# Kernel tuning notes

Measured on AMD Instinct MI355X. Metric: run time of the kernel, lower is better.

The kernel has to match this reference:

```python
import jax, jax.numpy as jnp
import numpy as np

D = 256
H = 8
HD = D // H
LN_EPS = 1e-5


def setup_inputs() -> dict:
    key = jax.random.key(0)
    ks = jax.random.split(key, 20)
    N = 768
    s = lambda *sh: 1.0 / np.sqrt(sh[-1])
    inp = {
        "features": jax.random.normal(ks[0], (N, D), jnp.float32),
        "boxes": jax.random.uniform(ks[1], (N, 4), jnp.float32),
        # MultiheadAttention params (torch layout: [out, in])
        "in_proj_w": jax.random.normal(ks[2], (3 * D, D), jnp.float32) * s(D),
        "in_proj_b": jnp.zeros((3 * D,), jnp.float32),
        "out_proj_w": jax.random.normal(ks[3], (D, D), jnp.float32) * s(D),
        "out_proj_b": jnp.zeros((D,), jnp.float32),
        # similarity_net params
        "w1": jax.random.normal(ks[4], (256, 3 * D + 3), jnp.float32) * s(3 * D + 3),
        "b1": jnp.zeros((256,), jnp.float32),
        "ln_g": jnp.ones((256,), jnp.float32),
        "ln_b": jnp.zeros((256,), jnp.float32),
        "w2": jax.random.normal(ks[5], (128, 256), jnp.float32) * s(256),
        "b2": jnp.zeros((128,), jnp.float32),
        "w3": jax.random.normal(ks[6], (64, 128), jnp.float32) * s(128),
        "b3": jnp.zeros((64,), jnp.float32),
        "w4": jax.random.normal(ks[7], (32, 64), jnp.float32) * s(64),
        "b4": jnp.zeros((32,), jnp.float32),
        "w5": jax.random.normal(ks[8], (1, 32), jnp.float32) * s(32),
        "b5": jnp.zeros((1,), jnp.float32),
    }
    return inp


def _mha(x, in_w, in_b, out_w, out_b):
    # x: [N, D]; torch nn.MultiheadAttention self-attention (eval mode)
    N = x.shape[0]
    qkv = x @ in_w.T + in_b                      # [N, 3D]
    q, k, v = jnp.split(qkv, 3, axis=-1)
    q = q.reshape(N, H, HD).transpose(1, 0, 2)   # [H, N, HD]
    k = k.reshape(N, H, HD).transpose(1, 0, 2)
    v = v.reshape(N, H, HD).transpose(1, 0, 2)
    scores = jnp.einsum("hnd,hmd->hnm", q, k) / np.sqrt(HD)
    attn = jax.nn.softmax(scores, axis=-1)
    o = jnp.einsum("hnm,hmd->hnd", attn, v)      # [H, N, HD]
    o = o.transpose(1, 0, 2).reshape(N, D)
    return o @ out_w.T + out_b


def reference(features, boxes, in_proj_w, in_proj_b, out_proj_w, out_proj_b,
              w1, b1, ln_g, ln_b, w2, b2, w3, b3, w4, b4, w5, b5):
    N = features.shape[0]
    att = _mha(features, in_proj_w, in_proj_b, out_proj_w, out_proj_b)  # [N, D]

    fi = jnp.broadcast_to(att[:, None, :], (N, N, D))
    fj = jnp.broadcast_to(att[None, :, :], (N, N, D))
    bi = boxes[:, None, :]
    bj = boxes[None, :, :]
    x_dist = jnp.abs(bi[:, :, 0] - bj[:, :, 0])
    y_diff = bi[:, :, 1] - bj[:, :, 1]
    spatial = jnp.stack([x_dist, jnp.abs(y_diff), y_diff], axis=-1)    # [N, N, 3]
    pairs = jnp.concatenate([fi, fj, fi * fj, spatial], axis=-1)       # [N, N, 3D+3]

    h = jax.nn.relu(pairs @ w1.T + b1)
    mu = jnp.mean(h, axis=-1, keepdims=True)
    var = jnp.var(h, axis=-1, keepdims=True)
    h = (h - mu) / jnp.sqrt(var + LN_EPS) * ln_g + ln_b
    h = jax.nn.relu(h @ w2.T + b2)
    h = jax.nn.relu(h @ w3.T + b3)
    h = jax.nn.relu(h @ w4.T + b4)
    logits = (h @ w5.T + b5)[..., 0]                                   # [N, N]

    eye = jnp.eye(N, dtype=logits.dtype)
    return logits * (1.0 - eye) - 1e9 * eye
```

## Files before the change

kernel.cpp:

```cpp
#include <hip/hip_runtime.h>


typedef __attribute__((ext_vector_type(8))) __bf16 bf16x8;
typedef __attribute__((ext_vector_type(4))) float f32x4;
typedef __attribute__((ext_vector_type(8))) int i32x8;

__device__ __forceinline__ float bf2f(unsigned short u) {
    return __uint_as_float(((unsigned int)u) << 16);
}
__device__ __forceinline__ unsigned short f2bf(float f) {
    union { __bf16 b; unsigned short u; } cv;
    cv.b = (__bf16)f;
    return cv.u;
}
__device__ __forceinline__ unsigned pk2(float lo, float hi) {
    return (unsigned)f2bf(lo) | ((unsigned)f2bf(hi) << 16);
}
__device__ __forceinline__ int pk4_fp8(float a, float b, float c, float d) {
    int w = __builtin_amdgcn_cvt_pk_fp8_f32(a, b, 0, false);
    w = __builtin_amdgcn_cvt_pk_fp8_f32(c, d, w, true);
    return w;
}
__device__ __forceinline__ unsigned char f2fp8(float v) {
    return (unsigned char)(__builtin_amdgcn_cvt_pk_fp8_f32(v, 0.f, 0, false) & 0xff);
}
__device__ __forceinline__ bf16x8 load8f_bf(const float* p) {
    float4 a = *reinterpret_cast<const float4*>(p);
    float4 b = *reinterpret_cast<const float4*>(p + 4);
    union { bf16x8 v; unsigned u[4]; } cv;
    cv.u[0] = pk2(a.x, a.y); cv.u[1] = pk2(a.z, a.w);
    cv.u[2] = pk2(b.x, b.y); cv.u[3] = pk2(b.z, b.w);
    return cv.v;
}
#define SC1 0x7F7F7F7F
#define MFMA_MX(a, b, c) __builtin_amdgcn_mfma_scale_f32_16x16x128_f8f6f4( \
        (a), (b), (c), 0, 0, 0, SC1, 0, SC1)

__global__ __launch_bounds__(256) void pack_all(
    const float* __restrict__ features, const float* __restrict__ in_proj_w,
    const float* __restrict__ in_proj_b, const float* __restrict__ out_proj_w,
    const float* __restrict__ w1, const float* __restrict__ w2,
    const float* __restrict__ w3, const float* __restrict__ w4,
    const float* __restrict__ b1, const float* __restrict__ ln_g,
    const float* __restrict__ ln_b, const float* __restrict__ b2,
    const float* __restrict__ out_proj_b,
    unsigned short* __restrict__ qkvb, unsigned short* __restrict__ Vt,
    unsigned short* __restrict__ WcatB,
    unsigned char* __restrict__ w1c_mx, unsigned char* __restrict__ w1t_f8,
    unsigned char* __restrict__ w2g_mx, unsigned char* __restrict__ w3_mx,
    unsigned char* __restrict__ w4_f8,
    float* __restrict__ bias768, float* __restrict__ c1, float* __restrict__ c2)
{
    const int blk = blockIdx.x;
    if (blk < 716) {
        int t = blk * 256 + threadIdx.x;
        if (t < 65536) {
            WcatB[t] = f2bf(out_proj_w[t]);
        } else if (t < 131072) {
            int u = t - 65536;
            int e = u & 31, lane = (u >> 5) & 63, f = u >> 11;
            int mt = f & 15, ks = f >> 4;
            int o = mt * 16 + (lane & 15);
            int k = ks * 128 + ((lane >> 4) & 3) * 32 + e;
            w1c_mx[u] = f2fp8(w1[o * 771 + 512 + k]);
        } else if (t < 139264) {
            int u = t - 131072;
            int e = u & 7, lane = (u >> 3) & 63, f = u >> 9;
            int o = f * 16 + (lane & 15);
            int k = ((lane >> 4) & 3) * 8 + e;
            float v = (k < 3) ? w1[o * 771 + 768 + k] : 0.f;
            w1t_f8[u] = f2fp8(v);
        } else if (t < 172032) {
            int u = t - 139264;
            int e = u & 31, lane = (u >> 5) & 63, f = u >> 11;
            int mt = f & 7, ks = f >> 3;
            int p = mt * 16 + (lane & 15);
            int k = ks * 128 + ((lane >> 4) & 3) * 32 + e;
            w2g_mx[u] = f2fp8(w2[p * 256 + k] * ln_g[k]);
        } else if (t < 180224) {
            int u = t - 172032;
            int e = u & 31, lane = (u >> 5) & 63, f = u >> 11;
            int o = f * 16 + (lane & 15);
            int k = ((lane >> 4) & 3) * 32 + e;
            w3_mx[u] = f2fp8(w3[o * 128 + k]);
        } else if (t < 182272) {
            int u = t - 180224;
            int e = u & 7, lane = (u >> 3) & 63, f = u >> 9;
            int l15 = lane & 15, quad = lane >> 4;
            int ct = f & 1, kc = f >> 1;
            int o = ct * 16 + l15, k = kc * 32 + quad * 8 + e;
            w4_f8[u] = f2fp8(w4[o * 64 + k]);
        } else if (t < 183040) {
            int n = t - 182272;
            if (n < 256) bias768[n] = out_proj_b[n];
            else {
                int m = n - 256;
                float s = 0.f;
                for (int d = 0; d < 256; d += 4) {
                    float4 ob = *reinterpret_cast<const float4*>(&out_proj_b[d]);
                    const float* wr = (m < 256) ? &w1[m * 771 + d]
                                                : &w1[(m - 256) * 771 + 256 + d];
                    float4 w = *reinterpret_cast<const float4*>(wr);
                    s += ob.x * w.x + ob.y * w.y + ob.z * w.z + ob.w * w.w;
                }
                bias768[n] = s + ((m < 256) ? b1[m] : 0.f);
            }
        } else if (t < 183168) {
            int p = t - 183040;
            float s2 = 0.f, s1 = 0.f;
            for (int k = 0; k < 256; k += 4) {
                float4 w = *reinterpret_cast<const float4*>(&w2[p * 256 + k]);
                float4 g = *reinterpret_cast<const float4*>(&ln_g[k]);
                float4 lb = *reinterpret_cast<const float4*>(&ln_b[k]);
                s2 += g.x * w.x + g.y * w.y + g.z * w.z + g.w * w.w;
                s1 += lb.x * w.x + lb.y * w.y + lb.z * w.z + lb.w * w.w;
            }
            c2[p] = s2;
            c1[p] = s1 + b2[p];
        }
    } else if (blk < 1228) {
        const int n = blk - 716, e = threadIdx.x;
        const float* wrow = (n < 256) ? &w1[n * 771] : &w1[(n - 256) * 771 + 256];
        float acc = 0.f;
        for (int d = 0; d < 256; d += 4) {
            float4 w = *reinterpret_cast<const float4*>(&wrow[d]);
            acc += w.x * out_proj_w[(d + 0) * 256 + e];
            acc += w.y * out_proj_w[(d + 1) * 256 + e];
            acc += w.z * out_proj_w[(d + 2) * 256 + e];
            acc += w.w * out_proj_w[(d + 3) * 256 + e];
        }
        WcatB[(256 + n) * 256 + e] = f2bf(acc);
    } else {
        const int q = blk - 1228;
        const int bm = q % 12, bn = q / 12;
        const int wv = threadIdx.x >> 6, lane = threadIdx.x & 63;
        const int l15 = lane & 15, quad = lane >> 4;
        const int row0 = bm * 64 + wv * 16;
        const int col0 = bn * 64;
        f32x4 acc[4] = {};
        for (int kc = 0; kc < 8; ++kc) {
            bf16x8 a = load8f_bf(&features[(row0 + l15) * 256 + kc * 32 + quad * 8]);
#pragma unroll
            for (int ct = 0; ct < 4; ++ct) {
                bf16x8 b = load8f_bf(&in_proj_w[(col0 + ct * 16 + l15) * 256 + kc * 32 + quad * 8]);
                acc[ct] = __builtin_amdgcn_mfma_f32_16x16x32_bf16(a, b, acc[ct], 0, 0, 0);
            }
        }
#pragma unroll
        for (int ct = 0; ct < 4; ++ct)
#pragma unroll
            for (int r = 0; r < 4; ++r) {
                int row = row0 + quad * 4 + r, col = col0 + ct * 16 + l15;
                float v = acc[ct][r] + in_proj_b[col];
                if (col < 512) qkvb[row * 768 + col] = f2bf(v);
                else           Vt[(col - 512) * 768 + row] = f2bf(v);
            }
    }
}

__global__ __launch_bounds__(256) void gemm_attab(
    const unsigned short* __restrict__ A, const unsigned short* __restrict__ W,
    const float* __restrict__ bias, float* __restrict__ att,
    float* __restrict__ AB)
{
    const int wv = threadIdx.x >> 6, lane = threadIdx.x & 63;
    const int l15 = lane & 15, quad = lane >> 4;
    const int row0 = blockIdx.x * 64 + wv * 16;
    const int col0 = blockIdx.y * 64;
    f32x4 acc[4] = {};
    for (int kc = 0; kc < 8; ++kc) {
        bf16x8 a = *reinterpret_cast<const bf16x8*>(&A[(row0 + l15) * 256 + kc * 32 + quad * 8]);
#pragma unroll
        for (int ct = 0; ct < 4; ++ct) {
            bf16x8 b = *reinterpret_cast<const bf16x8*>(&W[(col0 + ct * 16 + l15) * 256 + kc * 32 + quad * 8]);
            acc[ct] = __builtin_amdgcn_mfma_f32_16x16x32_bf16(a, b, acc[ct], 0, 0, 0);
        }
    }
#pragma unroll
    for (int ct = 0; ct < 4; ++ct)
#pragma unroll
        for (int r = 0; r < 4; ++r) {
            int row = row0 + quad * 4 + r, col = col0 + ct * 16 + l15;
            float v = acc[ct][r] + bias[col];
            if (col < 256) att[row * 256 + col] = v;
            else           AB[row * 512 + (col - 256)] = v;
        }
}

#define SP 776

__global__ __launch_bounds__(256) void attn_mfma(
    const unsigned short* __restrict__ qkvb, const unsigned short* __restrict__ Vt,
    unsigned short* __restrict__ Obf)
{
    __shared__ __align__(16) unsigned short smS[32 * SP];
    __shared__ float s_inv[32];
    const int h = blockIdx.x, q0 = blockIdx.y * 32, hb = h * 32;
    const int tid = threadIdx.x, wave = tid >> 6, lane = tid & 63;
    const int l15 = lane & 15, quad = lane >> 4;

    bf16x8 af[2];
#pragma unroll
    for (int mt = 0; mt < 2; ++mt)
        af[mt] = *reinterpret_cast<const bf16x8*>(&qkvb[(q0 + mt * 16 + l15) * 768 + hb + quad * 8]);
#pragma unroll
    for (int ct = 0; ct < 12; ++ct) {
        int n0 = wave * 192 + ct * 16;
        bf16x8 b = *reinterpret_cast<const bf16x8*>(&qkvb[(n0 + l15) * 768 + 256 + hb + quad * 8]);
#pragma unroll
        for (int mt = 0; mt < 2; ++mt) {
            f32x4 c = {};
            c = __builtin_amdgcn_mfma_f32_16x16x32_bf16(af[mt], b, c, 0, 0, 0);
#pragma unroll
            for (int r = 0; r < 4; ++r)
                smS[(mt * 16 + quad * 4 + r) * SP + n0 + l15] =
                    f2bf(c[r] * 0.17677669529663689f);
        }
    }
    __syncthreads();

    {
        const int row = tid >> 3, part = tid & 7;
        unsigned short* rp = &smS[row * SP + part * 96];
        float ls = 0.f;
#pragma unroll
        for (int c8 = 0; c8 < 12; ++c8) {
            uint4 v = *reinterpret_cast<const uint4*>(&rp[c8 * 8]);
            const unsigned short* pe = reinterpret_cast<const unsigned short*>(&v);
            unsigned short o8[8];
#pragma unroll
            for (int e = 0; e < 8; ++e) {
                float ev = __expf(bf2f(pe[e]));
                ls += ev;
                o8[e] = f2bf(ev);
            }
            *reinterpret_cast<uint4*>(&rp[c8 * 8]) = *reinterpret_cast<const uint4*>(o8);
        }
        ls += __shfl_xor(ls, 1, 64);
        ls += __shfl_xor(ls, 2, 64);
        ls += __shfl_xor(ls, 4, 64);
        if (part == 0) s_inv[row] = 1.0f / ls;
    }
    __syncthreads();

    const int row0 = (wave >> 1) * 16, cg = wave & 1;
    f32x4 accp = {};
    for (int kc = 0; kc < 24; ++kc) {
        bf16x8 a = *reinterpret_cast<const bf16x8*>(&smS[(row0 + l15) * SP + kc * 32 + quad * 8]);
        bf16x8 b = *reinterpret_cast<const bf16x8*>(&Vt[(hb + cg * 16 + l15) * 768 + kc * 32 + quad * 8]);
        accp = __builtin_amdgcn_mfma_f32_16x16x32_bf16(a, b, accp, 0, 0, 0);
    }
#pragma unroll
    for (int r = 0; r < 4; ++r) {
        int rloc = row0 + quad * 4 + r;
        Obf[(q0 + rloc) * 256 + hb + cg * 16 + l15] = f2bf(accp[r] * s_inv[rloc]);
    }
}

__global__ __launch_bounds__(512, 2) void pair_mlp(
    const float* __restrict__ att, const float* __restrict__ AB,
    const unsigned char* __restrict__ w1c_mx, const unsigned char* __restrict__ w1t_f8,
    const unsigned char* __restrict__ w2g_mx, const unsigned char* __restrict__ w3_mx,
    const unsigned char* __restrict__ w4_f8,
    const float* __restrict__ boxes,
    const float* __restrict__ c1, const float* __restrict__ c2,
    const float* __restrict__ b3, const float* __restrict__ b4,
    const float* __restrict__ w5, const float* __restrict__ b5,
    float* __restrict__ out)
{
    __shared__ __align__(16) unsigned char smH[64 * 384];
    __shared__ __align__(16) unsigned char smH1[64 * 256];
    __shared__ __align__(16) unsigned char smH2[64 * 192];
    __shared__ __align__(16) unsigned char smH3[64 * 72];
    __shared__ float s_psum[64][8], s_pssq[64][8];
    __shared__ float s_mu[64], s_rs[64];
    __shared__ float s_l5[64][2];

    const int i    = blockIdx.x;
    const int j0   = blockIdx.y * 64;
    const int tid  = threadIdx.x;
    const int wave = tid >> 6;
    const int lane = tid & 63;
    const int l15  = lane & 15;
    const int quad = lane >> 4;

    {
        const int g = tid & 63;
        const int ch = g >> 2;
        float4 fi4 = *reinterpret_cast<const float4*>(&att[i * 256 + g * 4]);
#pragma unroll 4
        for (int it = 0; it < 8; ++it) {
            int r = (tid >> 6) + it * 8;
            float4 aj = *reinterpret_cast<const float4*>(&att[(j0 + r) * 256 + g * 4]);
            int cs = ch ^ (r & 15);
            *reinterpret_cast<int*>(&smH[r * 384 + cs * 16 + (g & 3) * 4]) =
                pk4_fp8(aj.x * fi4.x, aj.y * fi4.y, aj.z * fi4.z, aj.w * fi4.w);
        }
    }
    if (tid < 64) {
        int j = j0 + tid;
        float xd = fabsf(boxes[i * 4 + 0] - boxes[j * 4 + 0]);
        float yd = boxes[i * 4 + 1] - boxes[j * 4 + 1];
        unsigned char* tb = &smH[tid * 384 + 256 + (tid & 3) * 24];
        *reinterpret_cast<int*>(tb)      = pk4_fp8(xd, fabsf(yd), yd, 0.f);
        *reinterpret_cast<int*>(tb + 4)  = 0;
        *reinterpret_cast<long long*>(tb + 8)  = 0;
        *reinterpret_cast<long long*>(tb + 16) = 0;
        *reinterpret_cast<long long*>(tb + 24) = 0;
    }
    __syncthreads();

    f32x4 acc1[2][4] = {};
#pragma unroll
    for (int ks = 0; ks < 2; ++ks) {
        i32x8 a0 = *reinterpret_cast<const i32x8*>(&w1c_mx[((ks * 16 + wave * 2 + 0) * 64 + lane) * 32]);
        i32x8 a1 = *reinterpret_cast<const i32x8*>(&w1c_mx[((ks * 16 + wave * 2 + 1) * 64 + lane) * 32]);
        const int cb = ks * 8 + quad * 2;
#pragma unroll
        for (int nt = 0; nt < 4; ++nt) {
            const unsigned char* rp = &smH[(nt * 16 + l15) * 384];
            union { i32x8 v; uint4 q[2]; } b;
            b.q[0] = *reinterpret_cast<const uint4*>(rp + ((cb    ) ^ l15) * 16);
            b.q[1] = *reinterpret_cast<const uint4*>(rp + ((cb + 1) ^ l15) * 16);
            acc1[0][nt] = MFMA_MX(a0, b.v, acc1[0][nt]);
            acc1[1][nt] = MFMA_MX(a1, b.v, acc1[1][nt]);
        }
    }
    {
        long long a0 = *reinterpret_cast<const long long*>(&w1t_f8[((wave * 2 + 0) * 64 + lane) * 8]);
        long long a1 = *reinterpret_cast<const long long*>(&w1t_f8[((wave * 2 + 1) * 64 + lane) * 8]);
#pragma unroll
        for (int nt = 0; nt < 4; ++nt) {
            long long b = *reinterpret_cast<const long long*>(
                &smH[(nt * 16 + l15) * 384 + 256 + (l15 & 3) * 24 + quad * 8]);
            acc1[0][nt] = __builtin_amdgcn_mfma_f32_16x16x32_fp8_fp8(a0, b, acc1[0][nt], 0, 0, 0);
            acc1[1][nt] = __builtin_amdgcn_mfma_f32_16x16x32_fp8_fp8(a1, b, acc1[1][nt], 0, 0, 0);
        }
    }

    const int o0 = wave * 32;
    float vsum[4] = {}, vssq[4] = {};
#pragma unroll
    for (int mt = 0; mt < 2; ++mt) {
        int o = o0 + mt * 16 + quad * 4;
        float4 Ai = *reinterpret_cast<const float4*>(&AB[i * 512 + o]);
        float AiA[4] = {Ai.x, Ai.y, Ai.z, Ai.w};
#pragma unroll
        for (int nt = 0; nt < 4; ++nt) {
            int j = nt * 16 + l15;
            float4 Bj = *reinterpret_cast<const float4*>(&AB[(j0 + j) * 512 + 256 + o]);
            float BjA[4] = {Bj.x, Bj.y, Bj.z, Bj.w};
#pragma unroll
            for (int r = 0; r < 4; ++r) {
                float v = fmaxf(acc1[mt][nt][r] + AiA[r] + BjA[r], 0.f);
                acc1[mt][nt][r] = v;
                vsum[nt] += v; vssq[nt] += v * v;
            }
        }
    }
#pragma unroll
    for (int nt = 0; nt < 4; ++nt) {
        vsum[nt] += __shfl_xor(vsum[nt], 16, 64);
        vsum[nt] += __shfl_xor(vsum[nt], 32, 64);
        vssq[nt] += __shfl_xor(vssq[nt], 16, 64);
        vssq[nt] += __shfl_xor(vssq[nt], 32, 64);
    }
    if (quad == 0)
#pragma unroll
        for (int nt = 0; nt < 4; ++nt) {
            s_psum[nt * 16 + l15][wave] = vsum[nt];
            s_pssq[nt * 16 + l15][wave] = vssq[nt];
        }
#pragma unroll
    for (int mt = 0; mt < 2; ++mt) {
        const int ch = wave * 2 + mt;
#pragma unroll
        for (int nt = 0; nt < 4; ++nt) {
            int j = nt * 16 + l15;
            *reinterpret_cast<int*>(&smH1[j * 256 + (ch ^ l15) * 16 + quad * 4]) =
                pk4_fp8(acc1[mt][nt][0], acc1[mt][nt][1], acc1[mt][nt][2], acc1[mt][nt][3]);
        }
    }
    __syncthreads();
    if (wave == 0) {
        int j = lane;
        float sm = 0.f, sq = 0.f;
#pragma unroll
        for (int w = 0; w < 8; ++w) { sm += s_psum[j][w]; sq += s_pssq[j][w]; }
        sm *= (1.0f / 256.0f); sq *= (1.0f / 256.0f);
        s_mu[j] = sm;
        s_rs[j] = rsqrtf(sq - sm * sm + 1e-5f);
    }

    f32x4 acc2[4] = {};
#pragma unroll
    for (int ks = 0; ks < 2; ++ks) {
        i32x8 a = *reinterpret_cast<const i32x8*>(&w2g_mx[((ks * 8 + wave) * 64 + lane) * 32]);
        const int cb = ks * 8 + quad * 2;
#pragma unroll
        for (int nt = 0; nt < 4; ++nt) {
            const unsigned char* rp = &smH1[(nt * 16 + l15) * 256];
            union { i32x8 v; uint4 q[2]; } b;
            b.q[0] = *reinterpret_cast<const uint4*>(rp + ((cb    ) ^ l15) * 16);
            b.q[1] = *reinterpret_cast<const uint4*>(rp + ((cb + 1) ^ l15) * 16);
            acc2[nt] = MFMA_MX(a, b.v, acc2[nt]);
        }
    }
    __syncthreads();
    {
        int p = wave * 16 + quad * 4;
        float4 C1 = *reinterpret_cast<const float4*>(&c1[p]);
        float4 C2 = *reinterpret_cast<const float4*>(&c2[p]);
        float C1A[4] = {C1.x, C1.y, C1.z, C1.w};
        float C2A[4] = {C2.x, C2.y, C2.z, C2.w};
#pragma unroll
        for (int nt = 0; nt < 4; ++nt) {
            int j = nt * 16 + l15;
            float mu = s_mu[j], rs = s_rs[j];
            float vv[4];
#pragma unroll
            for (int r = 0; r < 4; ++r)
                vv[r] = fmaxf(rs * (acc2[nt][r] - mu * C2A[r]) + C1A[r], 0.f);
            *reinterpret_cast<int*>(&smH2[j * 192 + (wave ^ (l15 & 7)) * 16 + quad * 4]) =
                pk4_fp8(vv[0], vv[1], vv[2], vv[3]);
        }
    }
    __syncthreads();

    const int qt  = wave >> 1;
    const int jh2 = wave & 1;
    f32x4 acc3[2] = {};
    {
        i32x8 a = *reinterpret_cast<const i32x8*>(&w3_mx[(qt * 64 + lane) * 32]);
        const int cb = quad * 2;
#pragma unroll
        for (int ntl = 0; ntl < 2; ++ntl) {
            int j = (jh2 * 2 + ntl) * 16 + l15;
            const unsigned char* rp = &smH2[j * 192];
            union { i32x8 v; uint4 q[2]; } b;
            b.q[0] = *reinterpret_cast<const uint4*>(rp + ((cb    ) ^ (l15 & 7)) * 16);
            b.q[1] = *reinterpret_cast<const uint4*>(rp + ((cb + 1) ^ (l15 & 7)) * 16);
            acc3[ntl] = MFMA_MX(a, b.v, acc3[ntl]);
        }
    }
    {
        int q = qt * 16 + quad * 4;
        float4 B3 = *reinterpret_cast<const float4*>(&b3[q]);
        float B3A[4] = {B3.x, B3.y, B3.z, B3.w};
#pragma unroll
        for (int ntl = 0; ntl < 2; ++ntl) {
            int j = (jh2 * 2 + ntl) * 16 + l15;
            float vv[4];
#pragma unroll
            for (int r = 0; r < 4; ++r)
                vv[r] = fmaxf(acc3[ntl][r] + B3A[r], 0.f);
            *reinterpret_cast<int*>(&smH3[j * 72 + q]) = pk4_fp8(vv[0], vv[1], vv[2], vv[3]);
        }
    }
    __syncthreads();

    const int mt4 = wave & 1;
    const int jq  = wave >> 1;
    f32x4 acc4 = {};
#pragma unroll
    for (int kc = 0; kc < 2; ++kc) {
        long long a = *reinterpret_cast<const long long*>(&w4_f8[((kc * 2 + mt4) * 64 + lane) * 8]);
        int j = jq * 16 + l15;
        long long b = *reinterpret_cast<const long long*>(&smH3[j * 72 + kc * 32 + quad * 8]);
        acc4 = __builtin_amdgcn_mfma_f32_16x16x32_fp8_fp8(a, b, acc4, 0, 0, 0);
    }
    {
        int o4 = mt4 * 16 + quad * 4;
        float4 B4 = *reinterpret_cast<const float4*>(&b4[o4]);
        float4 W5 = *reinterpret_cast<const float4*>(&w5[o4]);
        float B4A[4] = {B4.x, B4.y, B4.z, B4.w};
        float W5A[4] = {W5.x, W5.y, W5.z, W5.w};
        float part = 0.f;
#pragma unroll
        for (int r = 0; r < 4; ++r)
            part += fmaxf(acc4[r] + B4A[r], 0.f) * W5A[r];
        part += __shfl_xor(part, 16, 64);
        part += __shfl_xor(part, 32, 64);
        if (quad == 0)
            s_l5[jq * 16 + l15][mt4] = part;
    }
    __syncthreads();
    if (tid < 64) {
        int j = j0 + tid;
        float v = s_l5[tid][0] + s_l5[tid][1] + b5[0];
        out[i * 768 + j] = (j == i) ? -1.0e9f : v;
    }
}

extern "C" void kernel_launch(void* const* d_in, const int* in_sizes, int n_in,
                              void* d_out, int out_size, void* d_ws, size_t ws_size,
                              hipStream_t stream)
{
    const float* features   = (const float*)d_in[0];
    const float* boxes      = (const float*)d_in[1];
    const float* in_proj_w  = (const float*)d_in[2];
    const float* in_proj_b  = (const float*)d_in[3];
    const float* out_proj_w = (const float*)d_in[4];
    const float* out_proj_b = (const float*)d_in[5];
    const float* w1  = (const float*)d_in[6];
    const float* b1  = (const float*)d_in[7];
    const float* ln_g = (const float*)d_in[8];
    const float* ln_b = (const float*)d_in[9];
    const float* w2  = (const float*)d_in[10];
    const float* b2  = (const float*)d_in[11];
    const float* w3  = (const float*)d_in[12];
    const float* b3  = (const float*)d_in[13];
    const float* w4  = (const float*)d_in[14];
    const float* b4  = (const float*)d_in[15];
    const float* w5  = (const float*)d_in[16];
    const float* b5  = (const float*)d_in[17];
    float* out = (float*)d_out;

    char* p = (char*)d_ws;
    unsigned short* qkvb  = (unsigned short*)p; p += 768 * 768 * 2;
    unsigned short* Vt    = (unsigned short*)p; p += 256 * 768 * 2;
    unsigned short* Obf   = (unsigned short*)p; p += 768 * 256 * 2;
    unsigned short* WcatB = (unsigned short*)p; p += 196608 * 2;
    float* att = (float*)p; p += 768 * 256 * 4;
    float* AB  = (float*)p; p += 768 * 512 * 4;
    unsigned char* w1c_mx = (unsigned char*)p; p += 65536;
    unsigned char* w1t_f8 = (unsigned char*)p; p += 8192;
    unsigned char* w2g_mx = (unsigned char*)p; p += 32768;
    unsigned char* w3_mx  = (unsigned char*)p; p += 8192;
    unsigned char* w4_f8  = (unsigned char*)p; p += 2048;
    float* bias768 = (float*)p; p += 768 * 4;
    float* c1v     = (float*)p; p += 128 * 4;
    float* c2v     = (float*)p; p += 128 * 4;

    pack_all<<<dim3(1372), dim3(256), 0, stream>>>(features, in_proj_w,
        in_proj_b, out_proj_w, w1, w2, w3, w4, b1, ln_g, ln_b, b2, out_proj_b,
        qkvb, Vt, WcatB, w1c_mx, w1t_f8, w2g_mx, w3_mx, w4_f8,
        bias768, c1v, c2v);
    attn_mfma<<<dim3(8, 24), dim3(256), 0, stream>>>(qkvb, Vt, Obf);
    gemm_attab<<<dim3(12, 12), dim3(256), 0, stream>>>(Obf, WcatB, bias768,
        att, AB);
    pair_mlp<<<dim3(768, 12), dim3(512), 0, stream>>>(att, AB,
        w1c_mx, w1t_f8, w2g_mx, w3_mx, w4_f8, boxes, c1v, c2v,
        b3, b4, w5, b5, out);
}
```

Before: 283.1 us.

## Restructure pair MLP so each wave owns 32 pairs end-to-end without block syncs

The pair MLP kernel now runs 128-thread blocks in which each wave computes the full four-layer MLP for its own 32 j-columns. The layer-1 B operands are built directly in registers from global att instead of being staged in shared memory, and LayerNorm statistics are reduced inside the wave with shuffles. Only small per-wave shared buffers remain for the intermediate layers, which removes all __syncthreads and most LDS traffic. The cost is that every wave reloads the full weight matrices (more global/L2 traffic per pair), keeps larger accumulator arrays that raise register pressure, and issues redundant att loads per lane.

```diff
diff --git a/kernel.cpp b/kernel.cpp
--- a/kernel.cpp
+++ b/kernel.cpp
@@ -257,7 +257,7 @@
     }
 }
 
-__global__ __launch_bounds__(512, 2) void pair_mlp(
+__global__ __launch_bounds__(128, 3) void pair_mlp(
     const float* __restrict__ att, const float* __restrict__ AB,
     const unsigned char* __restrict__ w1c_mx, const unsigned char* __restrict__ w1t_f8,
     const unsigned char* __restrict__ w2g_mx, const unsigned char* __restrict__ w3_mx,
@@ -268,227 +268,215 @@
     const float* __restrict__ w5, const float* __restrict__ b5,
     float* __restrict__ out)
 {
-    __shared__ __align__(16) unsigned char smH[64 * 384];
-    __shared__ __align__(16) unsigned char smH1[64 * 256];
-    __shared__ __align__(16) unsigned char smH2[64 * 192];
-    __shared__ __align__(16) unsigned char smH3[64 * 72];
-    __shared__ float s_psum[64][8], s_pssq[64][8];
-    __shared__ float s_mu[64], s_rs[64];
-    __shared__ float s_l5[64][2];
-
-    const int i    = blockIdx.x;
-    const int j0   = blockIdx.y * 64;
-    const int tid  = threadIdx.x;
-    const int wave = tid >> 6;
-    const int lane = tid & 63;
-    const int l15  = lane & 15;
-    const int quad = lane >> 4;
-
+    __shared__ __align__(16) unsigned char smPool[2][8192];
+    const int tid = threadIdx.x, wave = tid >> 6, lane = tid & 63;
+    const int l15 = lane & 15, quad = lane >> 4;
+    const int i = blockIdx.x;
+    const int j0w = blockIdx.y * 64 + wave * 32;
+
+    unsigned char* const h1 = smPool[wave];
+    unsigned char* const h2 = smPool[wave];
+    unsigned char* const h3 = smPool[wave] + 4096;
+
+    i32x8 bf[2][2];
+    long long tf[2];
+#pragma unroll
+    for (int ks = 0; ks < 2; ++ks) {
+        const int bk = ks * 128 + quad * 32;
+        float4 fi[8];
+#pragma unroll
+        for (int c = 0; c < 8; ++c)
+            fi[c] = *reinterpret_cast<const float4*>(&att[i * 256 + bk + c * 4]);
+#pragma unroll
+        for (int g = 0; g < 2; ++g) {
+            const int j = j0w + g * 16 + l15;
+            union { i32x8 v; int w[8]; } u;
+#pragma unroll
+            for (int c = 0; c < 8; ++c) {
+                float4 fj = *reinterpret_cast<const float4*>(&att[j * 256 + bk + c * 4]);
+                u.w[c] = pk4_fp8(fi[c].x * fj.x, fi[c].y * fj.y,
+                                 fi[c].z * fj.z, fi[c].w * fj.w);
+            }
+            bf[g][ks] = u.v;
+        }
+    }
     {
-        const int g = tid & 63;
-        const int ch = g >> 2;
-        float4 fi4 = *reinterpret_cast<const float4*>(&att[i * 256 + g * 4]);
-#pragma unroll 4
-        for (int it = 0; it < 8; ++it) {
-            int r = (tid >> 6) + it * 8;
-            float4 aj = *reinterpret_cast<const float4*>(&att[(j0 + r) * 256 + g * 4]);
-            int cs = ch ^ (r & 15);
-            *reinterpret_cast<int*>(&smH[r * 384 + cs * 16 + (g & 3) * 4]) =
-                pk4_fp8(aj.x * fi4.x, aj.y * fi4.y, aj.z * fi4.z, aj.w * fi4.w);
-        }
-    }
-    if (tid < 64) {
-        int j = j0 + tid;
-        float xd = fabsf(boxes[i * 4 + 0] - boxes[j * 4 + 0]);
-        float yd = boxes[i * 4 + 1] - boxes[j * 4 + 1];
-        unsigned char* tb = &smH[tid * 384 + 256 + (tid & 3) * 24];
-        *reinterpret_cast<int*>(tb)      = pk4_fp8(xd, fabsf(yd), yd, 0.f);
-        *reinterpret_cast<int*>(tb + 4)  = 0;
-        *reinterpret_cast<long long*>(tb + 8)  = 0;
-        *reinterpret_cast<long long*>(tb + 16) = 0;
-        *reinterpret_cast<long long*>(tb + 24) = 0;
-    }
-    __syncthreads();
-
-    f32x4 acc1[2][4] = {};
-#pragma unroll
-    for (int ks = 0; ks < 2; ++ks) {
-        i32x8 a0 = *reinterpret_cast<const i32x8*>(&w1c_mx[((ks * 16 + wave * 2 + 0) * 64 + lane) * 32]);
-        i32x8 a1 = *reinterpret_cast<const i32x8*>(&w1c_mx[((ks * 16 + wave * 2 + 1) * 64 + lane) * 32]);
-        const int cb = ks * 8 + quad * 2;
-#pragma unroll
-        for (int nt = 0; nt < 4; ++nt) {
-            const unsigned char* rp = &smH[(nt * 16 + l15) * 384];
+        float bi0 = boxes[i * 4 + 0], bi1 = boxes[i * 4 + 1];
+#pragma unroll
+        for (int g = 0; g < 2; ++g) {
+            int j = j0w + g * 16 + l15;
+            float xd = fabsf(bi0 - boxes[j * 4 + 0]);
+            float yd = bi1 - boxes[j * 4 + 1];
+            int lo = pk4_fp8(xd, fabsf(yd), yd, 0.f);
+            tf[g] = (quad == 0) ? (long long)(unsigned)lo : 0LL;
+        }
+    }
+
+    float vsA = 0.f, vsB = 0.f, vqA = 0.f, vqB = 0.f;
+#pragma unroll
+    for (int h = 0; h < 2; ++h) {
+        f32x4 acc[8][2] = {};
+#pragma unroll
+        for (int ks = 0; ks < 2; ++ks)
+#pragma unroll
+            for (int m = 0; m < 8; ++m) {
+                i32x8 a = *reinterpret_cast<const i32x8*>(
+                    &w1c_mx[((ks * 16 + h * 8 + m) * 64 + lane) * 32]);
+                acc[m][0] = MFMA_MX(a, bf[0][ks], acc[m][0]);
+                acc[m][1] = MFMA_MX(a, bf[1][ks], acc[m][1]);
+            }
+#pragma unroll
+        for (int m = 0; m < 8; ++m) {
+            long long a = *reinterpret_cast<const long long*>(
+                &w1t_f8[((h * 8 + m) * 64 + lane) * 8]);
+            acc[m][0] = __builtin_amdgcn_mfma_f32_16x16x32_fp8_fp8(a, tf[0], acc[m][0], 0, 0, 0);
+            acc[m][1] = __builtin_amdgcn_mfma_f32_16x16x32_fp8_fp8(a, tf[1], acc[m][1], 0, 0, 0);
+        }
+#pragma unroll
+        for (int m = 0; m < 8; ++m) {
+            const int o = h * 128 + m * 16 + quad * 4;
+            float4 Ai = *reinterpret_cast<const float4*>(&AB[i * 512 + o]);
+            float AiA[4] = {Ai.x, Ai.y, Ai.z, Ai.w};
+#pragma unroll
+            for (int g = 0; g < 2; ++g) {
+                int j = j0w + g * 16 + l15;
+                float4 Bj = *reinterpret_cast<const float4*>(&AB[j * 512 + 256 + o]);
+                float BjA[4] = {Bj.x, Bj.y, Bj.z, Bj.w};
+                float vv[4];
+#pragma unroll
+                for (int r = 0; r < 4; ++r) {
+                    float v = fmaxf(acc[m][g][r] + AiA[r] + BjA[r], 0.f);
+                    vv[r] = v;
+                    if (g == 0) { vsA += v; vqA += v * v; }
+                    else        { vsB += v; vqB += v * v; }
+                }
+                *reinterpret_cast<int*>(&h1[(g * 16 + l15) * 256 +
+                    (((h * 8 + m) ^ l15) * 16) + quad * 4]) =
+                    pk4_fp8(vv[0], vv[1], vv[2], vv[3]);
+            }
+        }
+    }
+    float mu[2], rs[2];
+    {
+        vsA += __shfl_xor(vsA, 16, 64); vsA += __shfl_xor(vsA, 32, 64);
+        vqA += __shfl_xor(vqA, 16, 64); vqA += __shfl_xor(vqA, 32, 64);
+        vsB += __shfl_xor(vsB, 16, 64); vsB += __shfl_xor(vsB, 32, 64);
+        vqB += __shfl_xor(vqB, 16, 64); vqB += __shfl_xor(vqB, 32, 64);
+        mu[0] = vsA * (1.0f / 256.0f);
+        rs[0] = rsqrtf(vqA * (1.0f / 256.0f) - mu[0] * mu[0] + 1e-5f);
+        mu[1] = vsB * (1.0f / 256.0f);
+        rs[1] = rsqrtf(vqB * (1.0f / 256.0f) - mu[1] * mu[1] + 1e-5f);
+    }
+
+    i32x8 b2f[2][2];
+#pragma unroll
+    for (int g = 0; g < 2; ++g)
+#pragma unroll
+        for (int ks = 0; ks < 2; ++ks) {
+            const unsigned char* rp = &h1[(g * 16 + l15) * 256];
+            const int cb = ks * 8 + quad * 2;
             union { i32x8 v; uint4 q[2]; } b;
             b.q[0] = *reinterpret_cast<const uint4*>(rp + ((cb    ) ^ l15) * 16);
             b.q[1] = *reinterpret_cast<const uint4*>(rp + ((cb + 1) ^ l15) * 16);
-            acc1[0][nt] = MFMA_MX(a0, b.v, acc1[0][nt]);
-            acc1[1][nt] = MFMA_MX(a1, b.v, acc1[1][nt]);
-        }
-    }
-    {
-        long long a0 = *reinterpret_cast<const long long*>(&w1t_f8[((wave * 2 + 0) * 64 + lane) * 8]);
-        long long a1 = *reinterpret_cast<const long long*>(&w1t_f8[((wave * 2 + 1) * 64 + lane) * 8]);
-#pragma unroll
-        for (int nt = 0; nt < 4; ++nt) {
+            b2f[g][ks] = b.v;
+        }
+    f32x4 acc2[8][2] = {};
+#pragma unroll
+    for (int ks = 0; ks < 2; ++ks)
+#pragma unroll
+        for (int m = 0; m < 8; ++m) {
+            i32x8 a = *reinterpret_cast<const i32x8*>(
+                &w2g_mx[((ks * 8 + m) * 64 + lane) * 32]);
+            acc2[m][0] = MFMA_MX(a, b2f[0][ks], acc2[m][0]);
+            acc2[m][1] = MFMA_MX(a, b2f[1][ks], acc2[m][1]);
+        }
+#pragma unroll
+    for (int m = 0; m < 8; ++m) {
+        const int p = m * 16 + quad * 4;
+        float4 C1v = *reinterpret_cast<const float4*>(&c1[p]);
+        float4 C2v = *reinterpret_cast<const float4*>(&c2[p]);
+        float C1A[4] = {C1v.x, C1v.y, C1v.z, C1v.w};
+        float C2A[4] = {C2v.x, C2v.y, C2v.z, C2v.w};
+#pragma unroll
+        for (int g = 0; g < 2; ++g) {
+            float vv[4];
+#pragma unroll
+            for (int r = 0; r < 4; ++r)
+                vv[r] = fmaxf(rs[g] * (acc2[m][g][r] - mu[g] * C2A[r]) + C1A[r], 0.f);
+            *reinterpret_cast<int*>(&h2[(g * 16 + l15) * 128 +
+                ((m ^ (l15 & 7)) * 16) + quad * 4]) =
+                pk4_fp8(vv[0], vv[1], vv[2], vv[3]);
+        }
+    }
+
+    i32x8 b3f[2];
+#pragma unroll
+    for (int g = 0; g < 2; ++g) {
+        const unsigned char* rp = &h2[(g * 16 + l15) * 128];
+        const int cb = quad * 2;
+        union { i32x8 v; uint4 q[2]; } b;
+        b.q[0] = *reinterpret_cast<const uint4*>(rp + ((cb    ) ^ (l15 & 7)) * 16);
+        b.q[1] = *reinterpret_cast<const uint4*>(rp + ((cb + 1) ^ (l15 & 7)) * 16);
+        b3f[g] = b.v;
+    }
+    f32x4 acc3[4][2] = {};
+#pragma unroll
+    for (int m = 0; m < 4; ++m) {
+        i32x8 a = *reinterpret_cast<const i32x8*>(&w3_mx[(m * 64 + lane) * 32]);
+        acc3[m][0] = MFMA_MX(a, b3f[0], acc3[m][0]);
+        acc3[m][1] = MFMA_MX(a, b3f[1], acc3[m][1]);
+    }
+#pragma unroll
+    for (int m = 0; m < 4; ++m) {
+        const int qo = m * 16 + quad * 4;
+        float4 B3 = *reinterpret_cast<const float4*>(&b3[qo]);
+        float B3A[4] = {B3.x, B3.y, B3.z, B3.w};
+#pragma unroll
+        for (int g = 0; g < 2; ++g) {
+            float vv[4];
+#pragma unroll
+            for (int r = 0; r < 4; ++r)
+                vv[r] = fmaxf(acc3[m][g][r] + B3A[r], 0.f);
+            *reinterpret_cast<int*>(&h3[(g * 16 + l15) * 80 + qo]) =
+                pk4_fp8(vv[0], vv[1], vv[2], vv[3]);
+        }
+    }
+
+    f32x4 acc4[2][2] = {};
+#pragma unroll
+    for (int g = 0; g < 2; ++g)
+#pragma unroll
+        for (int kc = 0; kc < 2; ++kc) {
             long long b = *reinterpret_cast<const long long*>(
-                &smH[(nt * 16 + l15) * 384 + 256 + (l15 & 3) * 24 + quad * 8]);
-            acc1[0][nt] = __builtin_amdgcn_mfma_f32_16x16x32_fp8_fp8(a0, b, acc1[0][nt], 0, 0, 0);
-            acc1[1][nt] = __builtin_amdgcn_mfma_f32_16x16x32_fp8_fp8(a1, b, acc1[1][nt], 0, 0, 0);
-        }
-    }
-
-    const int o0 = wave * 32;
-    float vsum[4] = {}, vssq[4] = {};
-#pragma unroll
-    for (int mt = 0; mt < 2; ++mt) {
-        int o = o0 + mt * 16 + quad * 4;
-        float4 Ai = *reinterpret_cast<const float4*>(&AB[i * 512 + o]);
-        float AiA[4] = {Ai.x, Ai.y, Ai.z, Ai.w};
-#pragma unroll
-        for (int nt = 0; nt < 4; ++nt) {
-            int j = nt * 16 + l15;
-            float4 Bj = *reinterpret_cast<const float4*>(&AB[(j0 + j) * 512 + 256 + o]);
-            float BjA[4] = {Bj.x, Bj.y, Bj.z, Bj.w};
-#pragma unroll
-            for (int r = 0; r < 4; ++r) {
-                float v = fmaxf(acc1[mt][nt][r] + AiA[r] + BjA[r], 0.f);
-                acc1[mt][nt][r] = v;
-                vsum[nt] += v; vssq[nt] += v * v;
-            }
-        }
-    }
-#pragma unroll
-    for (int nt = 0; nt < 4; ++nt) {
-        vsum[nt] += __shfl_xor(vsum[nt], 16, 64);
-        vsum[nt] += __shfl_xor(vsum[nt], 32, 64);
-        vssq[nt] += __shfl_xor(vssq[nt], 16, 64);
-        vssq[nt] += __shfl_xor(vssq[nt], 32, 64);
-    }
-    if (quad == 0)
-#pragma unroll
-        for (int nt = 0; nt < 4; ++nt) {
-            s_psum[nt * 16 + l15][wave] = vsum[nt];
-            s_pssq[nt * 16 + l15][wave] = vssq[nt];
-        }
-#pragma unroll
-    for (int mt = 0; mt < 2; ++mt) {
-        const int ch = wave * 2 + mt;
-#pragma unroll
-        for (int nt = 0; nt < 4; ++nt) {
-            int j = nt * 16 + l15;
-            *reinterpret_cast<int*>(&smH1[j * 256 + (ch ^ l15) * 16 + quad * 4]) =
-                pk4_fp8(acc1[mt][nt][0], acc1[mt][nt][1], acc1[mt][nt][2], acc1[mt][nt][3]);
-        }
-    }
-    __syncthreads();
-    if (wave == 0) {
-        int j = lane;
-        float sm = 0.f, sq = 0.f;
-#pragma unroll
-        for (int w = 0; w < 8; ++w) { sm += s_psum[j][w]; sq += s_pssq[j][w]; }
-        sm *= (1.0f / 256.0f); sq *= (1.0f / 256.0f);
-        s_mu[j] = sm;
-        s_rs[j] = rsqrtf(sq - sm * sm + 1e-5f);
-    }
-
-    f32x4 acc2[4] = {};
-#pragma unroll
-    for (int ks = 0; ks < 2; ++ks) {
-        i32x8 a = *reinterpret_cast<const i32x8*>(&w2g_mx[((ks * 8 + wave) * 64 + lane) * 32]);
-        const int cb = ks * 8 + quad * 2;
-#pragma unroll
-        for (int nt = 0; nt < 4; ++nt) {
-            const unsigned char* rp = &smH1[(nt * 16 + l15) * 256];
-            union { i32x8 v; uint4 q[2]; } b;
-            b.q[0] = *reinterpret_cast<const uint4*>(rp + ((cb    ) ^ l15) * 16);
-            b.q[1] = *reinterpret_cast<const uint4*>(rp + ((cb + 1) ^ l15) * 16);
-            acc2[nt] = MFMA_MX(a, b.v, acc2[nt]);
-        }
-    }
-    __syncthreads();
-    {
-        int p = wave * 16 + quad * 4;
-        float4 C1 = *reinterpret_cast<const float4*>(&c1[p]);
-        float4 C2 = *reinterpret_cast<const float4*>(&c2[p]);
-        float C1A[4] = {C1.x, C1.y, C1.z, C1.w};
-        float C2A[4] = {C2.x, C2.y, C2.z, C2.w};
-#pragma unroll
-        for (int nt = 0; nt < 4; ++nt) {
-            int j = nt * 16 + l15;
-            float mu = s_mu[j], rs = s_rs[j];
-            float vv[4];
-#pragma unroll
-            for (int r = 0; r < 4; ++r)
-                vv[r] = fmaxf(rs * (acc2[nt][r] - mu * C2A[r]) + C1A[r], 0.f);
-            *reinterpret_cast<int*>(&smH2[j * 192 + (wave ^ (l15 & 7)) * 16 + quad * 4]) =
-                pk4_fp8(vv[0], vv[1], vv[2], vv[3]);
-        }
-    }
-    __syncthreads();
-
-    const int qt  = wave >> 1;
-    const int jh2 = wave & 1;
-    f32x4 acc3[2] = {};
-    {
-        i32x8 a = *reinterpret_cast<const i32x8*>(&w3_mx[(qt * 64 + lane) * 32]);
-        const int cb = quad * 2;
-#pragma unroll
-        for (int ntl = 0; ntl < 2; ++ntl) {
-            int j = (jh2 * 2 + ntl) * 16 + l15;
-            const unsigned char* rp = &smH2[j * 192];
-            union { i32x8 v; uint4 q[2]; } b;
-            b.q[0] = *reinterpret_cast<const uint4*>(rp + ((cb    ) ^ (l15 & 7)) * 16);
-            b.q[1] = *reinterpret_cast<const uint4*>(rp + ((cb + 1) ^ (l15 & 7)) * 16);
-            acc3[ntl] = MFMA_MX(a, b.v, acc3[ntl]);
-        }
-    }
-    {
-        int q = qt * 16 + quad * 4;
-        float4 B3 = *reinterpret_cast<const float4*>(&b3[q]);
-        float B3A[4] = {B3.x, B3.y, B3.z, B3.w};
-#pragma unroll
-        for (int ntl = 0; ntl < 2; ++ntl) {
-            int j = (jh2 * 2 + ntl) * 16 + l15;
-            float vv[4];
-#pragma unroll
-            for (int r = 0; r < 4; ++r)
-                vv[r] = fmaxf(acc3[ntl][r] + B3A[r], 0.f);
-            *reinterpret_cast<int*>(&smH3[j * 72 + q]) = pk4_fp8(vv[0], vv[1], vv[2], vv[3]);
-        }
-    }
-    __syncthreads();
-
-    const int mt4 = wave & 1;
-    const int jq  = wave >> 1;
-    f32x4 acc4 = {};
-#pragma unroll
-    for (int kc = 0; kc < 2; ++kc) {
-        long long a = *reinterpret_cast<const long long*>(&w4_f8[((kc * 2 + mt4) * 64 + lane) * 8]);
-        int j = jq * 16 + l15;
-        long long b = *reinterpret_cast<const long long*>(&smH3[j * 72 + kc * 32 + quad * 8]);
-        acc4 = __builtin_amdgcn_mfma_f32_16x16x32_fp8_fp8(a, b, acc4, 0, 0, 0);
-    }
-    {
-        int o4 = mt4 * 16 + quad * 4;
+                &h3[(g * 16 + l15) * 80 + kc * 32 + quad * 8]);
+#pragma unroll
+            for (int t = 0; t < 2; ++t) {
+                long long a = *reinterpret_cast<const long long*>(
+                    &w4_f8[((kc * 2 + t) * 64 + lane) * 8]);
+                acc4[t][g] = __builtin_amdgcn_mfma_f32_16x16x32_fp8_fp8(a, b, acc4[t][g], 0, 0, 0);
+            }
+        }
+    float partA = 0.f, partB = 0.f;
+#pragma unroll
+    for (int t = 0; t < 2; ++t) {
+        const int o4 = t * 16 + quad * 4;
         float4 B4 = *reinterpret_cast<const float4*>(&b4[o4]);
-        float4 W5 = *reinterpret_cast<const float4*>(&w5[o4]);
+        float4 W5v = *reinterpret_cast<const float4*>(&w5[o4]);
         float B4A[4] = {B4.x, B4.y, B4.z, B4.w};
-        float W5A[4] = {W5.x, W5.y, W5.z, W5.w};
-        float part = 0.f;
-#pragma unroll
-        for (int r = 0; r < 4; ++r)
-            part += fmaxf(acc4[r] + B4A[r], 0.f) * W5A[r];
-        part += __shfl_xor(part, 16, 64);
-        part += __shfl_xor(part, 32, 64);
-        if (quad == 0)
-            s_l5[jq * 16 + l15][mt4] = part;
-    }
-    __syncthreads();
-    if (tid < 64) {
-        int j = j0 + tid;
-        float v = s_l5[tid][0] + s_l5[tid][1] + b5[0];
-        out[i * 768 + j] = (j == i) ? -1.0e9f : v;
+        float W5A[4] = {W5v.x, W5v.y, W5v.z, W5v.w};
+#pragma unroll
+        for (int r = 0; r < 4; ++r) {
+            partA += fmaxf(acc4[t][0][r] + B4A[r], 0.f) * W5A[r];
+            partB += fmaxf(acc4[t][1][r] + B4A[r], 0.f) * W5A[r];
+        }
+    }
+    partA += __shfl_xor(partA, 16, 64); partA += __shfl_xor(partA, 32, 64);
+    partB += __shfl_xor(partB, 16, 64); partB += __shfl_xor(partB, 32, 64);
+    if (quad == 0) {
+        int jA = j0w + l15;
+        int jB = j0w + 16 + l15;
+        out[i * 768 + jA] = (jA == i) ? -1.0e9f : partA + b5[0];
+        out[i * 768 + jB] = (jB == i) ? -1.0e9f : partB + b5[0];
     }
 }
 
@@ -539,7 +527,7 @@
     attn_mfma<<<dim3(8, 24), dim3(256), 0, stream>>>(qkvb, Vt, Obf);
     gemm_attab<<<dim3(12, 12), dim3(256), 0, stream>>>(Obf, WcatB, bias768,
         att, AB);
-    pair_mlp<<<dim3(768, 12), dim3(512), 0, stream>>>(att, AB,
+    pair_mlp<<<dim3(768, 12), dim3(128), 0, stream>>>(att, AB,
         w1c_mx, w1t_f8, w2g_mx, w3_mx, w4_f8, boxes, c1v, c2v,
         b3, b4, w5, b5, out);
 }
```

Result: slower. 377.0 us (+33.2%).
